# Kernel optimization log

Hardware: AMD Instinct MI355X
Metric: run time of the kernel (lower is better)

Reference implementation:

```python
import jax, jax.numpy as jnp
import numpy as np

# ---- static dims (match TextMMadapter / Hydra(d_model=128, d_state=16, d_conv=7, expand=2)) ----
HID = 4096          # LLM hidden size
DM = 128            # adapter bottleneck / hydra d_model
DIN = 2 * DM        # d_inner = expand * d_model = 256
DST = 16            # d_state
HD = 64             # headdim (Mamba2/Hydra default)
NH = DIN // HD      # nheads = 4
DCONV = 7
CONV_DIM = DIN + 2 * DST            # 288
DIN_PROJ = 2 * DIN + 2 * DST + 2 * NH  # 552
SEQ, BATCH = 2048, 4


def setup_inputs() -> dict:
    key = jax.random.key(0)
    ks = jax.random.split(key, 12)
    rn = lambda k, shape, s=0.02: jax.random.normal(k, shape, jnp.float32) * s
    dt = jnp.exp(jax.random.uniform(ks[5], (NH,), jnp.float32, np.log(1e-3), np.log(1e-1)))
    return dict(
        x=jax.random.normal(ks[0], (SEQ, BATCH, HID), jnp.float32),
        w_down=rn(ks[1], (DM, HID)), b_down=jnp.zeros((DM,), jnp.float32),
        w_up=rn(ks[2], (HID, DM)), b_up=jnp.zeros((HID,), jnp.float32),
        gate1=jnp.asarray(0.6, jnp.float32),
        hy_in_w=rn(ks[3], (DIN_PROJ, DM)),
        hy_conv_w=rn(ks[4], (CONV_DIM, 1, DCONV), 0.2),
        hy_conv_b=jnp.zeros((CONV_DIM,), jnp.float32),
        hy_dt_bias=jnp.log(jnp.expm1(dt)),               # inverse softplus of dt init
        hy_A_log=jnp.log(jax.random.uniform(ks[6], (NH,), jnp.float32, 1.0, 16.0)),
        hy_D=jnp.ones((NH,), jnp.float32),
        hy_fcD_w=rn(ks[7], (NH, DIN)),
        hy_norm_w=jnp.ones((DIN,), jnp.float32),
        hy_out_w=rn(ks[8], (DM, DIN)),
    )


def _causal_conv(x, w, b):
    # depthwise causal conv1d; x: (b,l,c), w: (c,1,k)
    y = jax.lax.conv_general_dilated(
        jnp.transpose(x, (0, 2, 1)), w, (1,), [(DCONV - 1, 0)],
        feature_group_count=CONV_DIM, dimension_numbers=("NCH", "OIH", "NCH"))
    return jnp.transpose(y, (0, 2, 1)) + b


def _ssm_scan(x, dt, A, B, C):
    # selective scan: h_t = exp(dt_t A) h_{t-1} + dt_t B_t x_t ; y_t = C_t . h_t
    # x:(b,l,h,p) dt:(b,l,h) A:(h,) B,C:(b,l,n)
    dA = jnp.exp(dt * A)            # (b,l,h)
    dBx = dt[..., None] * x         # (b,l,h,p)

    def step(h, t):
        dA_t, dBx_t, B_t, C_t = t
        h = dA_t[:, :, None, None] * h + dBx_t[..., None] * B_t[:, None, None, :]
        y = jnp.einsum("bhpn,bn->bhp", h, C_t)
        return h, y

    h0 = jnp.zeros((x.shape[0], NH, HD, DST), x.dtype)
    _, ys = jax.lax.scan(step, h0, (jnp.moveaxis(dA, 1, 0), jnp.moveaxis(dBx, 1, 0),
                                    jnp.moveaxis(B, 1, 0), jnp.moveaxis(C, 1, 0)))
    return jnp.moveaxis(ys, 0, 1)   # (b,l,h,p)


def _hydra(u, in_w, conv_w, conv_b, dt_bias, A_log, D, fcD_w, norm_w, out_w):
    b, l, _ = u.shape
    zxbcdt = u @ in_w.T                                   # (b,l,552)
    z = zxbcdt[..., :DIN]
    xBC = zxbcdt[..., DIN:DIN + CONV_DIM]
    dt2 = zxbcdt[..., DIN + CONV_DIM:]
    dt_fw = jax.nn.softplus(dt2[..., :NH] + dt_bias)
    dt_bw = jax.nn.softplus(jnp.flip(dt2[..., NH:], 1) + dt_bias)
    xBC = jax.nn.silu(_causal_conv(xBC, conv_w, conv_b))
    xs = xBC[..., :DIN]
    Bm = xBC[..., DIN:DIN + DST]
    Cm = xBC[..., DIN + DST:]
    A = -jnp.exp(A_log)
    x4 = xs.reshape(b, l, NH, HD)
    y_fw = _ssm_scan(x4, dt_fw, A, Bm, Cm).reshape(b, l, DIN)
    y_bw = jnp.flip(_ssm_scan(jnp.flip(x4, 1), dt_bw, A, jnp.flip(Bm, 1), jnp.flip(Cm, 1)).reshape(b, l, DIN), 1)
    zero = jnp.zeros((b, 1, DIN), u.dtype)
    # quasiseparable mixer: strictly-causal fw + strictly-anticausal bw + data-dependent diagonal
    y = jnp.concatenate([zero, y_fw[:, :-1]], 1) + jnp.concatenate([y_bw[:, 1:], zero], 1)
    y = y + xs * jnp.repeat(xs @ fcD_w.T + D, HD, axis=-1)
    yz = y * jax.nn.silu(z)                               # gated RMSNorm (norm after gate)
    y = yz * jax.lax.rsqrt(jnp.mean(jnp.square(yz), -1, keepdims=True) + 1e-5) * norm_w
    return y @ out_w.T


def reference(x, w_down, b_down, w_up, b_up, gate1, hy_in_w, hy_conv_w, hy_conv_b,
              hy_dt_bias, hy_A_log, hy_D, hy_fcD_w, hy_norm_w, hy_out_w):
    x_init = x                                            # (S,B,HID)
    h = x @ w_down.T + b_down                             # (S,B,128)
    h = jnp.transpose(h, (1, 0, 2))                       # (B,S,128)
    h = jax.nn.gelu(h, approximate=False)
    xmid = h
    hp = (hy_in_w, hy_conv_w, hy_conv_b, hy_dt_bias, hy_A_log, hy_D, hy_fcD_w, hy_norm_w, hy_out_w)
    h = _hydra(h, *hp)
    h = _hydra(h, *hp)
    alpha = jax.nn.sigmoid(gate1)
    h = alpha * xmid + (1.0 - alpha) * h
    h = xmid + h
    h = h @ w_up.T + b_up                                 # (B,S,HID)
    return x_init + jnp.transpose(h, (1, 0, 2))
```

## Files before the change

kernel.cpp:

```cpp
#include <hip/hip_runtime.h>
#include <hip/hip_bf16.h>
#include <math.h>

#define SEQL 2048
#define NB   4
#define HID  4096
#define DM   128
#define DIN  256
#define DST  16
#define HD   64
#define NH   4
#define CONV_DIM 288
#define DPROJ 552
#define MROWS (SEQL*NB)
#define TCH 64
#define NCHUNK (SEQL/TCH)

typedef __attribute__((ext_vector_type(8))) short short8;
typedef __attribute__((ext_vector_type(4))) float f32x4;

__device__ __forceinline__ float siluf(float v){ return v / (1.f + expf(-v)); }
__device__ __forceinline__ float geluf(float v){ return 0.5f*v*(1.f + erff(v*0.70710678118654752f)); }
__device__ __forceinline__ float wave_sum(float v){
    #pragma unroll
    for (int o = 32; o > 0; o >>= 1) v += __shfl_xor(v, o, 64);
    return v;
}
__device__ __forceinline__ unsigned bfpack2(float a, float b){
    __hip_bfloat162 v = __float22bfloat162_rn(make_float2(a, b));
    return *reinterpret_cast<unsigned*>(&v);
}

__global__ __launch_bounds__(256) void k_prep_w(const float* __restrict__ w_down,
    const float* __restrict__ w_up, const float* __restrict__ in_w,
    const float* __restrict__ out_w,
    __hip_bfloat16* __restrict__ wd, __hip_bfloat16* __restrict__ wu,
    __hip_bfloat16* __restrict__ wi, __hip_bfloat16* __restrict__ wo)
{
    int idx = blockIdx.x*256 + threadIdx.x;
    if (idx < 524288) { wd[idx] = __float2bfloat16(w_down[idx]); return; }
    idx -= 524288;
    if (idx < 524288) { wu[idx] = __float2bfloat16(w_up[idx]); return; }
    idx -= 524288;
    if (idx < 71680) { wi[idx] = (idx < 552*128) ? __float2bfloat16(in_w[idx]) : __float2bfloat16(0.f); return; }
    idx -= 71680;
    if (idx < 32768) { wo[idx] = __float2bfloat16(out_w[idx]); }
}

__global__ __launch_bounds__(256) void k_down_mfma(const float* __restrict__ x,
    const __hip_bfloat16* __restrict__ wbf, float* __restrict__ partial)
{
    __shared__ __align__(16) short Abuf[64][72];
    __shared__ __align__(16) short Wbuf[128][72];
    const int tid = threadIdx.x;
    const int m0 = blockIdx.x * 64;
    const int ks = blockIdx.y;
    const int b  = m0 >> 11, l0 = m0 & 2047;
    const int lane = tid & 63, wv = tid >> 6;
    const int fr = lane & 15, q = lane >> 4;
    f32x4 acc[8];
    #pragma unroll
    for (int i = 0; i < 8; ++i) acc[i] = (f32x4){0.f,0.f,0.f,0.f};

    const int arow = tid >> 2, aseg = tid & 3;
    const int wrow = tid >> 1, wseg = tid & 1;

    for (int k0 = ks*2048; k0 < ks*2048 + 2048; k0 += 64) {
        const float4* ap = (const float4*)(x + (size_t)((l0 + arow)*NB + b)*HID + k0 + aseg*16);
        float4 f0 = ap[0], f1 = ap[1], f2 = ap[2], f3 = ap[3];
        const uint4* wp = (const uint4*)(wbf + (size_t)wrow*HID + k0 + wseg*32);
        uint4 w0 = wp[0], w1 = wp[1], w2 = wp[2], w3 = wp[3];
        uint4 pk0, pk1;
        pk0.x = bfpack2(f0.x,f0.y); pk0.y = bfpack2(f0.z,f0.w);
        pk0.z = bfpack2(f1.x,f1.y); pk0.w = bfpack2(f1.z,f1.w);
        pk1.x = bfpack2(f2.x,f2.y); pk1.y = bfpack2(f2.z,f2.w);
        pk1.z = bfpack2(f3.x,f3.y); pk1.w = bfpack2(f3.z,f3.w);
        uint4* adst = (uint4*)&Abuf[arow][aseg*16];
        adst[0] = pk0; adst[1] = pk1;
        uint4* wdst = (uint4*)&Wbuf[wrow][wseg*32];
        wdst[0] = w0; wdst[1] = w1; wdst[2] = w2; wdst[3] = w3;
        __syncthreads();
        #pragma unroll
        for (int kh = 0; kh < 2; ++kh) {
            short8 af = *reinterpret_cast<const short8*>(&Abuf[wv*16 + fr][kh*32 + q*8]);
            #pragma unroll
            for (int ns = 0; ns < 8; ++ns) {
                short8 bf = *reinterpret_cast<const short8*>(&Wbuf[ns*16 + fr][kh*32 + q*8]);
                acc[ns] = __builtin_amdgcn_mfma_f32_16x16x32_bf16(af, bf, acc[ns], 0, 0, 0);
            }
        }
        __syncthreads();
    }
    #pragma unroll
    for (int ns = 0; ns < 8; ++ns)
        #pragma unroll
        for (int r = 0; r < 4; ++r)
            partial[((size_t)ks*MROWS + m0 + wv*16 + q*4 + r)*DM + ns*16 + fr] = acc[ns][r];
}

__global__ __launch_bounds__(256) void k_down_fix(const float* __restrict__ partial,
    const float* __restrict__ bias, float* __restrict__ xmid,
    __hip_bfloat16* __restrict__ ubf)
{
    size_t i4 = ((size_t)blockIdx.x*256 + threadIdx.x)*4;
    int n = (int)(i4 & (DM-1));
    float4 p0 = *(const float4*)&partial[i4];
    float4 p1 = *(const float4*)&partial[(size_t)MROWS*DM + i4];
    float4 bv = *(const float4*)&bias[n];
    float4 v;
    v.x = geluf(p0.x + p1.x + bv.x);
    v.y = geluf(p0.y + p1.y + bv.y);
    v.z = geluf(p0.z + p1.z + bv.z);
    v.w = geluf(p0.w + p1.w + bv.w);
    *(float4*)&xmid[i4] = v;
    uint2 pk; pk.x = bfpack2(v.x, v.y); pk.y = bfpack2(v.z, v.w);
    *(uint2*)&ubf[i4] = pk;
}

__global__ __launch_bounds__(256) void k_proj_in(const __hip_bfloat16* __restrict__ ubf,
    const __hip_bfloat16* __restrict__ wbf, float* __restrict__ zx)
{
    __shared__ __align__(16) short Abuf[64][136];
    __shared__ __align__(16) short Wbuf[80][136];
    const int tid = threadIdx.x;
    const int m0 = blockIdx.x*64;
    const int n0 = blockIdx.y*80;
    for (int i = tid; i < 64*16; i += 256) {
        int r = i >> 4, s = i & 15;
        *(uint4*)&Abuf[r][s*8] = *(const uint4*)&ubf[(size_t)(m0+r)*DM + s*8];
    }
    for (int i = tid; i < 80*16; i += 256) {
        int r = i >> 4, s = i & 15;
        *(uint4*)&Wbuf[r][s*8] = *(const uint4*)&wbf[(size_t)(n0+r)*DM + s*8];
    }
    __syncthreads();
    const int lane = tid & 63, wv = tid >> 6, fr = lane & 15, q = lane >> 4;
    f32x4 acc[5];
    #pragma unroll
    for (int i = 0; i < 5; ++i) acc[i] = (f32x4){0.f,0.f,0.f,0.f};
    #pragma unroll
    for (int kt = 0; kt < 4; ++kt) {
        short8 af = *reinterpret_cast<const short8*>(&Abuf[wv*16 + fr][kt*32 + q*8]);
        #pragma unroll
        for (int ns = 0; ns < 5; ++ns) {
            short8 bf = *reinterpret_cast<const short8*>(&Wbuf[ns*16 + fr][kt*32 + q*8]);
            acc[ns] = __builtin_amdgcn_mfma_f32_16x16x32_bf16(af, bf, acc[ns], 0, 0, 0);
        }
    }
    #pragma unroll
    for (int ns = 0; ns < 5; ++ns) {
        int n = n0 + ns*16 + fr;
        if (n < DPROJ) {
            #pragma unroll
            for (int r = 0; r < 4; ++r)
                zx[(size_t)(m0 + wv*16 + q*4 + r)*DPROJ + n] = acc[ns][r];
        }
    }
}

__global__ __launch_bounds__(256) void k_proj_out(const __hip_bfloat16* __restrict__ ynbf,
    const __hip_bfloat16* __restrict__ wbf, float* __restrict__ h,
    __hip_bfloat16* __restrict__ ubf)
{
    __shared__ __align__(16) short Abuf[64][136];
    __shared__ __align__(16) short Wbuf[128][136];
    const int tid = threadIdx.x;
    const int m0 = blockIdx.x*64;
    const int lane = tid & 63, wv = tid >> 6, fr = lane & 15, q = lane >> 4;
    f32x4 acc[8];
    #pragma unroll
    for (int i = 0; i < 8; ++i) acc[i] = (f32x4){0.f,0.f,0.f,0.f};
    for (int kb = 0; kb < 2; ++kb) {
        if (kb) __syncthreads();
        for (int i = tid; i < 64*16; i += 256) {
            int r = i >> 4, s = i & 15;
            *(uint4*)&Abuf[r][s*8] = *(const uint4*)&ynbf[(size_t)(m0+r)*DIN + kb*128 + s*8];
        }
        for (int i = tid; i < 128*16; i += 256) {
            int r = i >> 4, s = i & 15;
            *(uint4*)&Wbuf[r][s*8] = *(const uint4*)&wbf[(size_t)r*DIN + kb*128 + s*8];
        }
        __syncthreads();
        #pragma unroll
        for (int kt = 0; kt < 4; ++kt) {
            short8 af = *reinterpret_cast<const short8*>(&Abuf[wv*16 + fr][kt*32 + q*8]);
            #pragma unroll
            for (int ns = 0; ns < 8; ++ns) {
                short8 bf = *reinterpret_cast<const short8*>(&Wbuf[ns*16 + fr][kt*32 + q*8]);
                acc[ns] = __builtin_amdgcn_mfma_f32_16x16x32_bf16(af, bf, acc[ns], 0, 0, 0);
            }
        }
    }
    #pragma unroll
    for (int ns = 0; ns < 8; ++ns)
        #pragma unroll
        for (int r = 0; r < 4; ++r) {
            int m = m0 + wv*16 + q*4 + r, n = ns*16 + fr;
            float v = acc[ns][r];
            h[(size_t)m*DM + n] = v;
            ubf[(size_t)m*DM + n] = __float2bfloat16(v);
        }
}

__global__ __launch_bounds__(256) void k_prep_up(const float* __restrict__ xmid,
    const float* __restrict__ h2, const float* __restrict__ gate1,
    __hip_bfloat16* __restrict__ hc)
{
    const float alpha = 1.f / (1.f + expf(-gate1[0]));
    size_t i4 = ((size_t)blockIdx.x*256 + threadIdx.x)*4;
    float4 a = *(const float4*)&xmid[i4];
    float4 b = *(const float4*)&h2[i4];
    float ca = 1.f + alpha, cb = 1.f - alpha;
    uint2 pk;
    pk.x = bfpack2(ca*a.x + cb*b.x, ca*a.y + cb*b.y);
    pk.y = bfpack2(ca*a.z + cb*b.z, ca*a.w + cb*b.w);
    *(uint2*)&hc[i4] = pk;
}

__global__ __launch_bounds__(256) void k_up_mfma(const __hip_bfloat16* __restrict__ hc,
    const __hip_bfloat16* __restrict__ wbf, const float* __restrict__ b_up,
    const float* __restrict__ x, float* __restrict__ out)
{
    __shared__ __align__(16) short Abuf[64][136];
    __shared__ __align__(16) short Wbuf[128][136];
    const int tid = threadIdx.x;
    const int m0 = blockIdx.x*64;
    const int n0 = blockIdx.y*128;
    for (int i = tid; i < 64*16; i += 256) {
        int r = i >> 4, s = i & 15;
        *(uint4*)&Abuf[r][s*8] = *(const uint4*)&hc[(size_t)(m0+r)*DM + s*8];
    }
    for (int i = tid; i < 128*16; i += 256) {
        int r = i >> 4, s = i & 15;
        *(uint4*)&Wbuf[r][s*8] = *(const uint4*)&wbf[(size_t)(n0+r)*DM + s*8];
    }
    __syncthreads();
    const int lane = tid & 63, wv = tid >> 6, fr = lane & 15, q = lane >> 4;
    f32x4 acc[8];
    #pragma unroll
    for (int i = 0; i < 8; ++i) acc[i] = (f32x4){0.f,0.f,0.f,0.f};
    #pragma unroll
    for (int kt = 0; kt < 4; ++kt) {
        short8 af = *reinterpret_cast<const short8*>(&Abuf[wv*16 + fr][kt*32 + q*8]);
        #pragma unroll
        for (int ns = 0; ns < 8; ++ns) {
            short8 bf = *reinterpret_cast<const short8*>(&Wbuf[ns*16 + fr][kt*32 + q*8]);
            acc[ns] = __builtin_amdgcn_mfma_f32_16x16x32_bf16(af, bf, acc[ns], 0, 0, 0);
        }
    }
    #pragma unroll
    for (int r = 0; r < 4; ++r) {
        int m = m0 + wv*16 + q*4 + r;
        int b = m >> 11, l = m & 2047;
        size_t rowbase = (size_t)(l*NB + b)*HID + n0;
        #pragma unroll
        for (int ns = 0; ns < 8; ++ns) {
            int n = ns*16 + fr;
            out[rowbase + n] = acc[ns][r] + b_up[n0 + n] + x[rowbase + n];
        }
    }
}

__global__ __launch_bounds__(256) void k_conv(const float* __restrict__ zx,
    const float* __restrict__ cw, const float* __restrict__ cb,
    float* __restrict__ xBC)
{
    int idx = blockIdx.x*256 + threadIdx.x;
    if (idx >= MROWS*CONV_DIM) return;
    int c = idx % CONV_DIM;
    int m = idx / CONV_DIM;
    int l = m & 2047, b = m >> 11;
    float acc = cb[c];
    #pragma unroll
    for (int k = 0; k < 7; ++k) {
        int l2 = l - 6 + k;
        if (l2 >= 0)
            acc = fmaf(zx[(size_t)(b*SEQL + l2)*DPROJ + DIN + c], cw[c*7 + k], acc);
    }
    xBC[(size_t)m*CONV_DIM + c] = siluf(acc);
}

__global__ __launch_bounds__(64) void k_scan_state(const float* __restrict__ zx,
    const float* __restrict__ xBC, const float* __restrict__ dt_bias,
    const float* __restrict__ A_log, float* __restrict__ Sbuf, float* __restrict__ Pbuf)
{
    const int bid = blockIdx.x;
    const int c   = bid & (NCHUNK-1);
    const int h   = (bid >> 5) & (NH-1);
    const int b   = (bid >> 7) & 3;
    const int dir = bid >> 9;
    const int tid = threadIdx.x;
    __shared__ float dA_s[TCH], dt_s[TCH];
    __shared__ float Xs[TCH][HD];
    __shared__ float Bs[TCH][DST];
    {
        const int kk = tid;
        const int l = dir ? (SEQL-1 - (c*TCH + kk)) : (c*TCH + kk);
        float dtraw = zx[(size_t)(b*SEQL + l)*DPROJ + 544 + dir*NH + h] + dt_bias[h];
        float dt = dtraw > 20.f ? dtraw : log1pf(expf(dtraw));
        dt_s[kk] = dt;
        dA_s[kk] = expf(dt * (-expf(A_log[h])));
    }
    __syncthreads();
    for (int i = tid; i < TCH*HD; i += 64) {
        int k2 = i >> 6, p = i & 63;
        int l2 = dir ? (SEQL-1 - (c*TCH + k2)) : (c*TCH + k2);
        Xs[k2][p] = dt_s[k2] * xBC[(size_t)(b*SEQL + l2)*CONV_DIM + h*HD + p];
    }
    for (int i = tid; i < TCH*DST; i += 64) {
        int k2 = i >> 4, n = i & 15;
        int l2 = dir ? (SEQL-1 - (c*TCH + k2)) : (c*TCH + k2);
        Bs[k2][n] = xBC[(size_t)(b*SEQL + l2)*CONV_DIM + DIN + n];
    }
    __syncthreads();
    const int pg = tid >> 2, ng = tid & 3;
    float s[4][4];
    #pragma unroll
    for (int i = 0; i < 4; ++i)
        #pragma unroll
        for (int j = 0; j < 4; ++j) s[i][j] = 0.f;
    for (int k2 = 0; k2 < TCH; ++k2) {
        float dAv = dA_s[k2];
        float4 xv = *(const float4*)&Xs[k2][pg*4];
        float4 bv = *(const float4*)&Bs[k2][ng*4];
        float xa[4] = {xv.x, xv.y, xv.z, xv.w};
        float ba[4] = {bv.x, bv.y, bv.z, bv.w};
        #pragma unroll
        for (int i = 0; i < 4; ++i)
            #pragma unroll
            for (int j = 0; j < 4; ++j)
                s[i][j] = fmaf(dAv, s[i][j], xa[i]*ba[j]);
    }
    size_t sb = (size_t)bid * 1024;
    #pragma unroll
    for (int i = 0; i < 4; ++i) {
        float4 v = {s[i][0], s[i][1], s[i][2], s[i][3]};
        *(float4*)&Sbuf[sb + (size_t)((pg*4+i)*16 + ng*4)] = v;
    }
    if (tid == 0) {
        float P = 1.f;
        for (int k2 = 0; k2 < TCH; ++k2) P *= dA_s[k2];
        Pbuf[bid] = P;
    }
}

__global__ __launch_bounds__(1024) void k_scan_combine(const float* __restrict__ Sbuf,
    const float* __restrict__ Pbuf, float* __restrict__ Hbuf)
{
    const int t = threadIdx.x;
    const size_t base = (size_t)blockIdx.x * NCHUNK;
    float carry = 0.f;
    for (int c = 0; c < NCHUNK; ++c) {
        size_t cb = (base + c) * 1024;
        Hbuf[cb + t] = carry;
        carry = fmaf(Pbuf[base + c], carry, Sbuf[cb + t]);
    }
}

__global__ __launch_bounds__(64) void k_scan_out(const float* __restrict__ zx,
    const float* __restrict__ xBC, const float* __restrict__ dt_bias,
    const float* __restrict__ A_log, const float* __restrict__ Hbuf,
    float* __restrict__ yfw, float* __restrict__ ybw)
{
    const int bid = blockIdx.x;
    const int c   = bid & (NCHUNK-1);
    const int h   = (bid >> 5) & (NH-1);
    const int b   = (bid >> 7) & 3;
    const int dir = bid >> 9;
    const int tid = threadIdx.x;
    __shared__ float dA_s[TCH], dt_s[TCH];
    __shared__ float Xs[TCH][HD];
    __shared__ float Bs[TCH][DST];
    __shared__ float Cs[TCH][DST];
    {
        const int kk = tid;
        const int l = dir ? (SEQL-1 - (c*TCH + kk)) : (c*TCH + kk);
        float dtraw = zx[(size_t)(b*SEQL + l)*DPROJ + 544 + dir*NH + h] + dt_bias[h];
        float dt = dtraw > 20.f ? dtraw : log1pf(expf(dtraw));
        dt_s[kk] = dt;
        dA_s[kk] = expf(dt * (-expf(A_log[h])));
    }
    __syncthreads();
    for (int i = tid; i < TCH*HD; i += 64) {
        int k2 = i >> 6, p = i & 63;
        int l2 = dir ? (SEQL-1 - (c*TCH + k2)) : (c*TCH + k2);
        Xs[k2][p] = dt_s[k2] * xBC[(size_t)(b*SEQL + l2)*CONV_DIM + h*HD + p];
    }
    for (int i = tid; i < TCH*DST; i += 64) {
        int k2 = i >> 4, n = i & 15;
        int l2 = dir ? (SEQL-1 - (c*TCH + k2)) : (c*TCH + k2);
        Bs[k2][n] = xBC[(size_t)(b*SEQL + l2)*CONV_DIM + DIN + n];
        Cs[k2][n] = xBC[(size_t)(b*SEQL + l2)*CONV_DIM + DIN + DST + n];
    }
    __syncthreads();
    const int pg = tid >> 2, ng = tid & 3;
    float s[4][4];
    size_t hb = (size_t)bid * 1024;
    #pragma unroll
    for (int i = 0; i < 4; ++i) {
        float4 v = *(const float4*)&Hbuf[hb + (size_t)((pg*4+i)*16 + ng*4)];
        s[i][0] = v.x; s[i][1] = v.y; s[i][2] = v.z; s[i][3] = v.w;
    }
    float* yout = dir ? ybw : yfw;
    for (int k2 = 0; k2 < TCH; ++k2) {
        float dAv = dA_s[k2];
        float4 xv = *(const float4*)&Xs[k2][pg*4];
        float4 bv = *(const float4*)&Bs[k2][ng*4];
        float4 cv = *(const float4*)&Cs[k2][ng*4];
        float xa[4] = {xv.x, xv.y, xv.z, xv.w};
        float ba[4] = {bv.x, bv.y, bv.z, bv.w};
        float ca[4] = {cv.x, cv.y, cv.z, cv.w};
        float y[4];
        #pragma unroll
        for (int i = 0; i < 4; ++i) {
            #pragma unroll
            for (int j = 0; j < 4; ++j)
                s[i][j] = fmaf(dAv, s[i][j], xa[i]*ba[j]);
            y[i] = s[i][0]*ca[0] + s[i][1]*ca[1] + s[i][2]*ca[2] + s[i][3]*ca[3];
        }
        #pragma unroll
        for (int i = 0; i < 4; ++i) {
            y[i] += __shfl_xor(y[i], 1, 64);
            y[i] += __shfl_xor(y[i], 2, 64);
        }
        if (ng == 0) {
            int l2 = dir ? (SEQL-1 - (c*TCH + k2)) : (c*TCH + k2);
            float4 v = {y[0], y[1], y[2], y[3]};
            *(float4*)&yout[(size_t)(b*SEQL + l2)*DIN + h*HD + pg*4] = v;
        }
    }
}

__global__ __launch_bounds__(256) void k_epi(const float* __restrict__ zx,
    const float* __restrict__ xBC, const float* __restrict__ yfw,
    const float* __restrict__ ybw, const float* __restrict__ fcD_w,
    const float* __restrict__ Dv, const float* __restrict__ norm_w,
    __hip_bfloat16* __restrict__ ynbf)
{
    const int m = blockIdx.x;
    const int l = m & (SEQL-1);
    const int d = threadIdx.x;
    const int lane = d & 63, wave = d >> 6;
    __shared__ float red[4][4];
    __shared__ float redq[4];
    float xs = xBC[(size_t)m*CONV_DIM + d];
    float yv = 0.f;
    if (l > 0)       yv += yfw[(size_t)(m-1)*DIN + d];
    if (l < SEQL-1)  yv += ybw[(size_t)(m+1)*DIN + d];
    float p0 = wave_sum(xs * fcD_w[0*DIN + d]);
    float p1 = wave_sum(xs * fcD_w[1*DIN + d]);
    float p2 = wave_sum(xs * fcD_w[2*DIN + d]);
    float p3 = wave_sum(xs * fcD_w[3*DIN + d]);
    if (lane == 0) { red[wave][0]=p0; red[wave][1]=p1; red[wave][2]=p2; red[wave][3]=p3; }
    __syncthreads();
    const int h = d >> 6;
    float scal = red[0][h] + red[1][h] + red[2][h] + red[3][h] + Dv[h];
    yv = fmaf(xs, scal, yv);
    float z  = zx[(size_t)m*DPROJ + d];
    float yz = yv * siluf(z);
    float q = wave_sum(yz*yz);
    if (lane == 0) redq[wave] = q;
    __syncthreads();
    float ms = (redq[0] + redq[1] + redq[2] + redq[3]) * (1.f/DIN);
    float r = rsqrtf(ms + 1e-5f);
    ynbf[(size_t)m*DIN + d] = __float2bfloat16(yz * r * norm_w[d]);
}

extern "C" void kernel_launch(void* const* d_in, const int* in_sizes, int n_in,
                              void* d_out, int out_size, void* d_ws, size_t ws_size,
                              hipStream_t stream)
{
    const float* x       = (const float*)d_in[0];
    const float* w_down  = (const float*)d_in[1];
    const float* b_down  = (const float*)d_in[2];
    const float* w_up    = (const float*)d_in[3];
    const float* b_up    = (const float*)d_in[4];
    const float* gate1   = (const float*)d_in[5];
    const float* in_w    = (const float*)d_in[6];
    const float* conv_w  = (const float*)d_in[7];
    const float* conv_b  = (const float*)d_in[8];
    const float* dt_bias = (const float*)d_in[9];
    const float* A_log   = (const float*)d_in[10];
    const float* Dv      = (const float*)d_in[11];
    const float* fcD_w   = (const float*)d_in[12];
    const float* norm_w  = (const float*)d_in[13];
    const float* out_w   = (const float*)d_in[14];
    float* out = (float*)d_out;
    float* ws  = (float*)d_ws;

    size_t off = 0;
    float* xmid = ws + off; off += (size_t)MROWS*DM;
    float* h1   = ws + off; off += (size_t)MROWS*DM;
    float* h2   = ws + off; off += (size_t)MROWS*DM;
    float* zx   = ws + off; off += (size_t)MROWS*DPROJ;
    float* xBC  = ws + off; off += (size_t)MROWS*CONV_DIM;
    float* yfw  = ws + off; off += (size_t)MROWS*DIN;
    float* ybw  = ws + off; off += (size_t)MROWS*DIN;
    float* Sbuf = ws + off; off += (size_t)1024*1024;
    float* Pbuf = ws + off; off += 1024;
    float* Hbuf = ws + off; off += (size_t)1024*1024;
    __hip_bfloat16* bfb = (__hip_bfloat16*)(ws + off);
    size_t bo = 0;
    __hip_bfloat16* wd_bf = bfb + bo; bo += 524288;
    __hip_bfloat16* wu_bf = bfb + bo; bo += 524288;
    __hip_bfloat16* wi_bf = bfb + bo; bo += 71680;
    __hip_bfloat16* wo_bf = bfb + bo; bo += 32768;
    __hip_bfloat16* u_bf  = bfb + bo; bo += (size_t)MROWS*DM;
    __hip_bfloat16* yn_bf = bfb + bo; bo += (size_t)MROWS*DIN;
    __hip_bfloat16* hc_bf = bfb + bo; bo += (size_t)MROWS*DM;
    float* partial = zx;

    k_prep_w<<<4504, 256, 0, stream>>>(w_down, w_up, in_w, out_w, wd_bf, wu_bf, wi_bf, wo_bf);

    dim3 gdown(MROWS/64, 2);
    k_down_mfma<<<gdown, 256, 0, stream>>>(x, wd_bf, partial);
    k_down_fix<<<MROWS*DM/1024, 256, 0, stream>>>(partial, b_down, xmid, u_bf);

    for (int pass = 0; pass < 2; ++pass) {
        float* hout = pass ? h2 : h1;
        dim3 gin(MROWS/64, 7);
        k_proj_in<<<gin, 256, 0, stream>>>(u_bf, wi_bf, zx);
        k_conv<<<(MROWS*CONV_DIM)/256, 256, 0, stream>>>(zx, conv_w, conv_b, xBC);
        k_scan_state<<<1024, 64, 0, stream>>>(zx, xBC, dt_bias, A_log, Sbuf, Pbuf);
        k_scan_combine<<<32, 1024, 0, stream>>>(Sbuf, Pbuf, Hbuf);
        k_scan_out<<<1024, 64, 0, stream>>>(zx, xBC, dt_bias, A_log, Hbuf, yfw, ybw);
        k_epi<<<MROWS, 256, 0, stream>>>(zx, xBC, yfw, ybw, fcD_w, Dv, norm_w, yn_bf);
        k_proj_out<<<MROWS/64, 256, 0, stream>>>(yn_bf, wo_bf, hout, u_bf);
    }

    k_prep_up<<<MROWS*DM/1024, 256, 0, stream>>>(xmid, h2, gate1, hc_bf);
    dim3 gup(MROWS/64, HID/128);
    k_up_mfma<<<gup, 256, 0, stream>>>(hc_bf, wu_bf, b_up, x, out);
}
```

Before: 523.4 us.

## Fuse chunked scan into one cooperative kernel and fold gate blend into proj_out

The three scan kernels (chunk state, sequential combine, output) become one cooperative kernel that uses two grid-wide syncs, so each chunk loads its X/B/C tiles once and two launches go away. The combine step is now spread over all 1024 blocks instead of 32 blocks of 1024 threads, and the xBC tile loads are vectorised to float4. The alpha blend that produced hc is moved into the second-pass proj_out epilogue, which removes the k_prep_up kernel and the fp32 h1/h2 writes. The cost is a dependence on cooperative launch: all 1024 blocks must be co-resident, and grid syncs have their own overhead.

```diff
diff --git a/kernel.cpp b/kernel.cpp
--- a/kernel.cpp
+++ b/kernel.cpp
@@ -1,6 +1,9 @@
 #include <hip/hip_runtime.h>
 #include <hip/hip_bf16.h>
+#include <hip/hip_cooperative_groups.h>
 #include <math.h>
+
+namespace cg = cooperative_groups;
 
 #define SEQL 2048
 #define NB   4
@@ -158,9 +161,11 @@
     }
 }
 
-__global__ __launch_bounds__(256) void k_proj_out(const __hip_bfloat16* __restrict__ ynbf,
-    const __hip_bfloat16* __restrict__ wbf, float* __restrict__ h,
-    __hip_bfloat16* __restrict__ ubf)
+template<int PASS>
+__global__ __launch_bounds__(256) void k_proj_out_t(const __hip_bfloat16* __restrict__ ynbf,
+    const __hip_bfloat16* __restrict__ wbf, const float* __restrict__ xmid,
+    const float* __restrict__ gate1,
+    __hip_bfloat16* __restrict__ ubf, __hip_bfloat16* __restrict__ hcbf)
 {
     __shared__ __align__(16) short Abuf[64][136];
     __shared__ __align__(16) short Wbuf[128][136];
@@ -191,30 +196,24 @@
             }
         }
     }
+    float ca = 0.f, cb = 0.f;
+    if (PASS == 1) {
+        float al = 1.f / (1.f + expf(-gate1[0]));
+        ca = 1.f + al; cb = 1.f - al;
+    }
     #pragma unroll
     for (int ns = 0; ns < 8; ++ns)
         #pragma unroll
         for (int r = 0; r < 4; ++r) {
             int m = m0 + wv*16 + q*4 + r, n = ns*16 + fr;
             float v = acc[ns][r];
-            h[(size_t)m*DM + n] = v;
-            ubf[(size_t)m*DM + n] = __float2bfloat16(v);
-        }
-}
-
-__global__ __launch_bounds__(256) void k_prep_up(const float* __restrict__ xmid,
-    const float* __restrict__ h2, const float* __restrict__ gate1,
-    __hip_bfloat16* __restrict__ hc)
-{
-    const float alpha = 1.f / (1.f + expf(-gate1[0]));
-    size_t i4 = ((size_t)blockIdx.x*256 + threadIdx.x)*4;
-    float4 a = *(const float4*)&xmid[i4];
-    float4 b = *(const float4*)&h2[i4];
-    float ca = 1.f + alpha, cb = 1.f - alpha;
-    uint2 pk;
-    pk.x = bfpack2(ca*a.x + cb*b.x, ca*a.y + cb*b.y);
-    pk.y = bfpack2(ca*a.z + cb*b.z, ca*a.w + cb*b.w);
-    *(uint2*)&hc[i4] = pk;
+            if (PASS == 0) {
+                ubf[(size_t)m*DM + n] = __float2bfloat16(v);
+            } else {
+                float xm = xmid[(size_t)m*DM + n];
+                hcbf[(size_t)m*DM + n] = __float2bfloat16(ca*xm + cb*v);
+            }
+        }
 }
 
 __global__ __launch_bounds__(256) void k_up_mfma(const __hip_bfloat16* __restrict__ hc,
@@ -280,86 +279,10 @@
     xBC[(size_t)m*CONV_DIM + c] = siluf(acc);
 }
 
-__global__ __launch_bounds__(64) void k_scan_state(const float* __restrict__ zx,
+__global__ __launch_bounds__(64) void k_scan_fused(const float* __restrict__ zx,
     const float* __restrict__ xBC, const float* __restrict__ dt_bias,
-    const float* __restrict__ A_log, float* __restrict__ Sbuf, float* __restrict__ Pbuf)
-{
-    const int bid = blockIdx.x;
-    const int c   = bid & (NCHUNK-1);
-    const int h   = (bid >> 5) & (NH-1);
-    const int b   = (bid >> 7) & 3;
-    const int dir = bid >> 9;
-    const int tid = threadIdx.x;
-    __shared__ float dA_s[TCH], dt_s[TCH];
-    __shared__ float Xs[TCH][HD];
-    __shared__ float Bs[TCH][DST];
-    {
-        const int kk = tid;
-        const int l = dir ? (SEQL-1 - (c*TCH + kk)) : (c*TCH + kk);
-        float dtraw = zx[(size_t)(b*SEQL + l)*DPROJ + 544 + dir*NH + h] + dt_bias[h];
-        float dt = dtraw > 20.f ? dtraw : log1pf(expf(dtraw));
-        dt_s[kk] = dt;
-        dA_s[kk] = expf(dt * (-expf(A_log[h])));
-    }
-    __syncthreads();
-    for (int i = tid; i < TCH*HD; i += 64) {
-        int k2 = i >> 6, p = i & 63;
-        int l2 = dir ? (SEQL-1 - (c*TCH + k2)) : (c*TCH + k2);
-        Xs[k2][p] = dt_s[k2] * xBC[(size_t)(b*SEQL + l2)*CONV_DIM + h*HD + p];
-    }
-    for (int i = tid; i < TCH*DST; i += 64) {
-        int k2 = i >> 4, n = i & 15;
-        int l2 = dir ? (SEQL-1 - (c*TCH + k2)) : (c*TCH + k2);
-        Bs[k2][n] = xBC[(size_t)(b*SEQL + l2)*CONV_DIM + DIN + n];
-    }
-    __syncthreads();
-    const int pg = tid >> 2, ng = tid & 3;
-    float s[4][4];
-    #pragma unroll
-    for (int i = 0; i < 4; ++i)
-        #pragma unroll
-        for (int j = 0; j < 4; ++j) s[i][j] = 0.f;
-    for (int k2 = 0; k2 < TCH; ++k2) {
-        float dAv = dA_s[k2];
-        float4 xv = *(const float4*)&Xs[k2][pg*4];
-        float4 bv = *(const float4*)&Bs[k2][ng*4];
-        float xa[4] = {xv.x, xv.y, xv.z, xv.w};
-        float ba[4] = {bv.x, bv.y, bv.z, bv.w};
-        #pragma unroll
-        for (int i = 0; i < 4; ++i)
-            #pragma unroll
-            for (int j = 0; j < 4; ++j)
-                s[i][j] = fmaf(dAv, s[i][j], xa[i]*ba[j]);
-    }
-    size_t sb = (size_t)bid * 1024;
-    #pragma unroll
-    for (int i = 0; i < 4; ++i) {
-        float4 v = {s[i][0], s[i][1], s[i][2], s[i][3]};
-        *(float4*)&Sbuf[sb + (size_t)((pg*4+i)*16 + ng*4)] = v;
-    }
-    if (tid == 0) {
-        float P = 1.f;
-        for (int k2 = 0; k2 < TCH; ++k2) P *= dA_s[k2];
-        Pbuf[bid] = P;
-    }
-}
-
-__global__ __launch_bounds__(1024) void k_scan_combine(const float* __restrict__ Sbuf,
-    const float* __restrict__ Pbuf, float* __restrict__ Hbuf)
-{
-    const int t = threadIdx.x;
-    const size_t base = (size_t)blockIdx.x * NCHUNK;
-    float carry = 0.f;
-    for (int c = 0; c < NCHUNK; ++c) {
-        size_t cb = (base + c) * 1024;
-        Hbuf[cb + t] = carry;
-        carry = fmaf(Pbuf[base + c], carry, Sbuf[cb + t]);
-    }
-}
-
-__global__ __launch_bounds__(64) void k_scan_out(const float* __restrict__ zx,
-    const float* __restrict__ xBC, const float* __restrict__ dt_bias,
-    const float* __restrict__ A_log, const float* __restrict__ Hbuf,
+    const float* __restrict__ A_log, float* __restrict__ Sbuf,
+    float* __restrict__ Pbuf, float* __restrict__ Hbuf,
     float* __restrict__ yfw, float* __restrict__ ybw)
 {
     const int bid = blockIdx.x;
@@ -381,24 +304,79 @@
         dA_s[kk] = expf(dt * (-expf(A_log[h])));
     }
     __syncthreads();
-    for (int i = tid; i < TCH*HD; i += 64) {
-        int k2 = i >> 6, p = i & 63;
+    #pragma unroll
+    for (int t = 0; t < 16; ++t) {
+        int k2 = t*4 + (tid >> 4);
+        int p4 = (tid & 15)*4;
         int l2 = dir ? (SEQL-1 - (c*TCH + k2)) : (c*TCH + k2);
-        Xs[k2][p] = dt_s[k2] * xBC[(size_t)(b*SEQL + l2)*CONV_DIM + h*HD + p];
-    }
-    for (int i = tid; i < TCH*DST; i += 64) {
-        int k2 = i >> 4, n = i & 15;
+        float4 v = *(const float4*)&xBC[(size_t)(b*SEQL + l2)*CONV_DIM + h*HD + p4];
+        float sc = dt_s[k2];
+        v.x *= sc; v.y *= sc; v.z *= sc; v.w *= sc;
+        *(float4*)&Xs[k2][p4] = v;
+    }
+    #pragma unroll
+    for (int t = 0; t < 4; ++t) {
+        int k2 = t*16 + (tid >> 2);
+        int n4 = (tid & 3)*4;
         int l2 = dir ? (SEQL-1 - (c*TCH + k2)) : (c*TCH + k2);
-        Bs[k2][n] = xBC[(size_t)(b*SEQL + l2)*CONV_DIM + DIN + n];
-        Cs[k2][n] = xBC[(size_t)(b*SEQL + l2)*CONV_DIM + DIN + DST + n];
+        *(float4*)&Bs[k2][n4] = *(const float4*)&xBC[(size_t)(b*SEQL + l2)*CONV_DIM + DIN + n4];
+        *(float4*)&Cs[k2][n4] = *(const float4*)&xBC[(size_t)(b*SEQL + l2)*CONV_DIM + DIN + DST + n4];
     }
     __syncthreads();
     const int pg = tid >> 2, ng = tid & 3;
     float s[4][4];
-    size_t hb = (size_t)bid * 1024;
+    #pragma unroll
+    for (int i = 0; i < 4; ++i)
+        #pragma unroll
+        for (int j = 0; j < 4; ++j) s[i][j] = 0.f;
+    for (int k2 = 0; k2 < TCH; ++k2) {
+        float dAv = dA_s[k2];
+        float4 xv = *(const float4*)&Xs[k2][pg*4];
+        float4 bv = *(const float4*)&Bs[k2][ng*4];
+        float xa[4] = {xv.x, xv.y, xv.z, xv.w};
+        float ba[4] = {bv.x, bv.y, bv.z, bv.w};
+        #pragma unroll
+        for (int i = 0; i < 4; ++i)
+            #pragma unroll
+            for (int j = 0; j < 4; ++j)
+                s[i][j] = fmaf(dAv, s[i][j], xa[i]*ba[j]);
+    }
+    const size_t sb = (size_t)bid * 1024;
     #pragma unroll
     for (int i = 0; i < 4; ++i) {
-        float4 v = *(const float4*)&Hbuf[hb + (size_t)((pg*4+i)*16 + ng*4)];
+        float4 v = {s[i][0], s[i][1], s[i][2], s[i][3]};
+        *(float4*)&Sbuf[sb + (size_t)((pg*4+i)*16 + ng*4)] = v;
+    }
+    {
+        float pv = dA_s[tid];
+        #pragma unroll
+        for (int o = 32; o > 0; o >>= 1) pv *= __shfl_xor(pv, o, 64);
+        if (tid == 0) Pbuf[bid] = pv;
+    }
+    cg::this_grid().sync();
+    {
+        const int gt = bid*64 + tid;
+        if (gt < 32*1024) {
+            const int g = gt >> 10, e = gt & 1023;
+            float sv[NCHUNK], pw[NCHUNK];
+            #pragma unroll
+            for (int cc = 0; cc < NCHUNK; ++cc)
+                sv[cc] = Sbuf[(size_t)(g*NCHUNK + cc)*1024 + e];
+            #pragma unroll
+            for (int cc = 0; cc < NCHUNK; ++cc)
+                pw[cc] = Pbuf[g*NCHUNK + cc];
+            float carry = 0.f;
+            #pragma unroll
+            for (int cc = 0; cc < NCHUNK; ++cc) {
+                Hbuf[(size_t)(g*NCHUNK + cc)*1024 + e] = carry;
+                carry = fmaf(pw[cc], carry, sv[cc]);
+            }
+        }
+    }
+    cg::this_grid().sync();
+    #pragma unroll
+    for (int i = 0; i < 4; ++i) {
+        float4 v = *(const float4*)&Hbuf[sb + (size_t)((pg*4+i)*16 + ng*4)];
         s[i][0] = v.x; s[i][1] = v.y; s[i][2] = v.z; s[i][3] = v.w;
     }
     float* yout = dir ? ybw : yfw;
@@ -490,8 +468,6 @@
 
     size_t off = 0;
     float* xmid = ws + off; off += (size_t)MROWS*DM;
-    float* h1   = ws + off; off += (size_t)MROWS*DM;
-    float* h2   = ws + off; off += (size_t)MROWS*DM;
     float* zx   = ws + off; off += (size_t)MROWS*DPROJ;
     float* xBC  = ws + off; off += (size_t)MROWS*CONV_DIM;
     float* yfw  = ws + off; off += (size_t)MROWS*DIN;
@@ -517,18 +493,23 @@
     k_down_fix<<<MROWS*DM/1024, 256, 0, stream>>>(partial, b_down, xmid, u_bf);
 
     for (int pass = 0; pass < 2; ++pass) {
-        float* hout = pass ? h2 : h1;
         dim3 gin(MROWS/64, 7);
         k_proj_in<<<gin, 256, 0, stream>>>(u_bf, wi_bf, zx);
         k_conv<<<(MROWS*CONV_DIM)/256, 256, 0, stream>>>(zx, conv_w, conv_b, xBC);
-        k_scan_state<<<1024, 64, 0, stream>>>(zx, xBC, dt_bias, A_log, Sbuf, Pbuf);
-        k_scan_combine<<<32, 1024, 0, stream>>>(Sbuf, Pbuf, Hbuf);
-        k_scan_out<<<1024, 64, 0, stream>>>(zx, xBC, dt_bias, A_log, Hbuf, yfw, ybw);
+        {
+            void* args[] = { (void*)&zx, (void*)&xBC, (void*)&dt_bias, (void*)&A_log,
+                             (void*)&Sbuf, (void*)&Pbuf, (void*)&Hbuf,
+                             (void*)&yfw, (void*)&ybw };
+            hipLaunchCooperativeKernel((void*)k_scan_fused, dim3(1024), dim3(64),
+                                       args, 0, stream);
+        }
         k_epi<<<MROWS, 256, 0, stream>>>(zx, xBC, yfw, ybw, fcD_w, Dv, norm_w, yn_bf);
-        k_proj_out<<<MROWS/64, 256, 0, stream>>>(yn_bf, wo_bf, hout, u_bf);
-    }
-
-    k_prep_up<<<MROWS*DM/1024, 256, 0, stream>>>(xmid, h2, gate1, hc_bf);
+        if (pass == 0)
+            k_proj_out_t<0><<<MROWS/64, 256, 0, stream>>>(yn_bf, wo_bf, xmid, gate1, u_bf, hc_bf);
+        else
+            k_proj_out_t<1><<<MROWS/64, 256, 0, stream>>>(yn_bf, wo_bf, xmid, gate1, u_bf, hc_bf);
+    }
+
     dim3 gup(MROWS/64, HID/128);
     k_up_mfma<<<gup, 256, 0, stream>>>(hc_bf, wu_bf, b_up, x, out);
 }
```

New measurement: 905.0 us. +72.9%, slower.
